# Performance work log

Hardware: AMD Instinct MI355X
Metric: run time of the kernel (lower is better)

Reference implementation:

```python
import jax, jax.numpy as jnp
import numpy as np


def setup_inputs() -> dict:
    key = jax.random.key(0)
    k = jax.random.split(key, 6)
    B, S, d, n = 4, 4096, 1024, 64
    x = jax.random.normal(k[0], (B, S, d), dtype=jnp.float32)
    gate_W = jax.random.normal(k[1], (d, n), dtype=jnp.float32) / np.sqrt(d).astype(np.float32)
    gate_b = jnp.full((n,), 3.0, dtype=jnp.float32)  # nn.init.constant_(gate_proj.bias, 3.0)
    B_W = jax.random.normal(k[2], (d, n), dtype=jnp.float32) / np.sqrt(d).astype(np.float32)
    C_W = jax.random.normal(k[3], (n, d), dtype=jnp.float32) / np.sqrt(n).astype(np.float32)
    out_W = jax.random.normal(k[4], (d, d), dtype=jnp.float32) / np.sqrt(d).astype(np.float32)
    mix_weight = jnp.eye(n, dtype=jnp.float32) + 0.01 * jax.random.normal(k[5], (n, n), dtype=jnp.float32)
    return {"x": x, "gate_W": gate_W, "gate_b": gate_b, "B_W": B_W,
            "C_W": C_W, "out_W": out_W, "mix_weight": mix_weight, "chunk_size": 16}


def _ssm_forward(x, gate_W, gate_b, B_W, C_W, out_W, mix_weight, chunk_size):
    Bb, S, d = x.shape
    n = gate_W.shape[1]
    C = chunk_size
    K = S // C  # seq_len chosen divisible by chunk_size -> F.pad path is a no-op
    # Vectorized per-timestep projections (done once for the whole sequence)
    gates = jax.nn.sigmoid(jnp.einsum('bsd,dn->bsn', x, gate_W) + gate_b)  # a_t in (0,1)
    b_all = jnp.einsum('bsd,dn->bsn', x, B_W)
    a_ch = gates.reshape(Bb, K, C, n).transpose(1, 2, 0, 3)  # (K, C, B, n)
    b_ch = b_all.reshape(Bb, K, C, n).transpose(1, 2, 0, 3)

    def chunk_step(h_prev, ab):
        a_c, b_c = ab  # each (C, B, n)
        def step(h, t):
            a_t, b_t = t
            h = a_t * h + b_t
            return h, h
        h_final, h_stack = jax.lax.scan(step, h_prev, (a_c, b_c))  # h_stack: (C, B, n)
        gate_prod = jnp.prod(a_c, axis=0)  # (B, n) cumulative diag gates
        # T_chunk = mix @ diag(gate_prod): T[b,i,j] = mix[i,j] * gate_prod[b,j]
        T = mix_weight[None, :, :] * gate_prod[:, None, :]
        Th = jnp.einsum('bij,bj->bi', T, h_prev)
        b_chunk = h_final - Th
        h_next = Th + b_chunk  # canonical inter-chunk propagation: T @ h_prev + b_chunk
        return h_next, h_stack

    h0 = jnp.zeros((Bb, n), dtype=x.dtype)
    _, h_all = jax.lax.scan(chunk_step, h0, (a_ch, b_ch))  # (K, C, B, n)
    h_seq = h_all.transpose(2, 0, 1, 3).reshape(Bb, S, n)
    y = jnp.einsum('bsn,nd->bsd', h_seq, C_W)
    out_gate = jax.nn.sigmoid(jnp.einsum('bsd,de->bse', x, out_W))
    return y * out_gate


def reference(x, gate_W, gate_b, B_W, C_W, out_W, mix_weight, chunk_size):
    return _ssm_forward(x, gate_W, gate_b, B_W, C_W, out_W, mix_weight, chunk_size)
```

## Files before the change

### kernel.cpp

```cpp
#include <hip/hip_runtime.h>
#include <stdint.h>

typedef __attribute__((ext_vector_type(8))) short short8;
typedef __attribute__((ext_vector_type(4))) float f32x4;
typedef __attribute__((ext_vector_type(4))) float f4;
typedef __attribute__((ext_vector_type(4))) unsigned short us4;

typedef unsigned short ushort_t;

__device__ __forceinline__ ushort_t f2bf(float f) {
    union { float f; uint32_t u; } c; c.f = f;
    uint32_t u = c.u;
    uint32_t r = u + 0x7fffu + ((u >> 16) & 1u);
    return (ushort_t)(r >> 16);
}
__device__ __forceinline__ float bf2f(ushort_t h) {
    union { uint32_t u; float f; } c; c.u = ((uint32_t)h) << 16;
    return c.f;
}

typedef const __attribute__((address_space(1))) unsigned int as1_uint;
typedef __attribute__((address_space(3))) unsigned int as3_uint;
__device__ __forceinline__ void gload_lds16(const void* g, void* l) {
    __builtin_amdgcn_global_load_lds((as1_uint*)g, (as3_uint*)l, 16, 0, 0);
}

#define SWIDX(r, c) ((r) * 64 + ((c) ^ (((r) & 7) << 3)))

__global__ void prep_weights(const float* __restrict__ gate_W, const float* __restrict__ B_W,
                             const float* __restrict__ C_W, const float* __restrict__ out_W,
                             ushort_t* __restrict__ W1t_hi, ushort_t* __restrict__ W1t_lo,
                             ushort_t* __restrict__ outWt, ushort_t* __restrict__ Ct)
{
    int idx = blockIdx.x * 256 + threadIdx.x;
    int stride = gridDim.x * 256;
    for (int i = idx; i < 1024 * 1024; i += stride) {
        int nn = i >> 10, kk = i & 1023;
        outWt[i] = f2bf(out_W[kk * 1024 + nn]);
    }
    for (int i = idx; i < 128 * 1024; i += stride) {
        int nn = i >> 10, kk = i & 1023;
        float v = (nn < 64) ? gate_W[kk * 64 + nn] : B_W[kk * 64 + (nn - 64)];
        ushort_t h = f2bf(v);
        W1t_hi[i] = h;
        W1t_lo[i] = f2bf(v - bf2f(h));
    }
    for (int i = idx; i < 1024 * 64; i += stride) {
        int nn = i >> 6, kk = i & 63;
        Ct[i] = f2bf(C_W[kk * 1024 + nn]);
    }
}

__global__ __launch_bounds__(256, 2)
void p1_kernel(const float* __restrict__ x,
               const ushort_t* __restrict__ W1t_hi, const ushort_t* __restrict__ W1t_lo,
               ushort_t* __restrict__ x_hi, float* __restrict__ Zpart)
{
    __shared__ ushort_t Ash[128 * 64];
    __shared__ ushort_t Asl[128 * 64];
    __shared__ ushort_t Bsh[64 * 64];
    __shared__ ushort_t Bsl[64 * 64];

    const int tid = threadIdx.x;
    const int wave = tid >> 6, lane = tid & 63;
    const int wm = wave >> 1, wn = wave & 1;
    const int s0 = blockIdx.x * 64;
    const int kc = blockIdx.y;

    f32x4 acc[4][2];
#pragma unroll
    for (int i = 0; i < 4; i++)
#pragma unroll
        for (int j = 0; j < 2; j++) { f32x4 z = {0.f,0.f,0.f,0.f}; acc[i][j] = z; }

    for (int kt = 0; kt < 8; ++kt) {
        const int k0 = kc * 512 + kt * 64;
#pragma unroll
        for (int p = 0; p < 4; ++p) {
            int c = p * 256 + wave * 64 + lane;
            int row = c >> 3, col = (c & 7) * 8;
            gload_lds16(W1t_hi + (size_t)row * 1024 + k0 + col,
                        &Ash[(p * 256 + wave * 64) * 8]);
            gload_lds16(W1t_lo + (size_t)row * 1024 + k0 + col,
                        &Asl[(p * 256 + wave * 64) * 8]);
        }
#pragma unroll
        for (int p = 0; p < 4; ++p) {
            int f = tid + p * 256;
            int row = f >> 4, col = (f & 15) * 4;
            f4 v = *(const f4*)(x + (size_t)(s0 + row) * 1024 + k0 + col);
            us4 hi, lo;
#pragma unroll
            for (int j = 0; j < 4; j++) {
                ushort_t h = f2bf(v[j]);
                hi[j] = h;
                lo[j] = f2bf(v[j] - bf2f(h));
            }
            *(us4*)&Bsh[row * 64 + col] = hi;
            *(us4*)&Bsl[row * 64 + col] = lo;
            *(us4*)(x_hi + (size_t)(s0 + row) * 1024 + k0 + col) = hi;
        }
        __syncthreads();
#pragma unroll
        for (int kk = 0; kk < 2; ++kk) {
            const int kb = kk * 32 + (lane >> 4) * 8;
            short8 ah[4], al[4], bh[2], bl[2];
#pragma unroll
            for (int fm = 0; fm < 4; fm++) {
                int r = wm * 64 + fm * 16 + (lane & 15);
                ah[fm] = *(const short8*)&Ash[r * 64 + kb];
                al[fm] = *(const short8*)&Asl[r * 64 + kb];
            }
#pragma unroll
            for (int fn = 0; fn < 2; fn++) {
                int r = wn * 32 + fn * 16 + (lane & 15);
                bh[fn] = *(const short8*)&Bsh[r * 64 + kb];
                bl[fn] = *(const short8*)&Bsl[r * 64 + kb];
            }
#pragma unroll
            for (int fm = 0; fm < 4; fm++)
#pragma unroll
                for (int fn = 0; fn < 2; fn++) {
                    acc[fm][fn] = __builtin_amdgcn_mfma_f32_16x16x32_bf16(ah[fm], bh[fn], acc[fm][fn], 0, 0, 0);
                    acc[fm][fn] = __builtin_amdgcn_mfma_f32_16x16x32_bf16(al[fm], bh[fn], acc[fm][fn], 0, 0, 0);
                    acc[fm][fn] = __builtin_amdgcn_mfma_f32_16x16x32_bf16(ah[fm], bl[fn], acc[fm][fn], 0, 0, 0);
                }
        }
        __syncthreads();
    }
#pragma unroll
    for (int fm = 0; fm < 4; fm++) {
#pragma unroll
        for (int fn = 0; fn < 2; fn++) {
            int scol = s0 + wn * 32 + fn * 16 + (lane & 15);
            int b = scol >> 12, sb = scol & 4095;
            int nbase = wm * 64 + fm * 16 + ((lane >> 4) << 2);
#pragma unroll
            for (int r = 0; r < 4; r++) {
                Zpart[((size_t)kc * 512 + b * 128 + nbase + r) * 4096 + sb] = acc[fm][fn][r];
            }
        }
    }
}

__global__ __launch_bounds__(256)
void scan_kernel(const float* __restrict__ Zpart, const float* __restrict__ gate_b,
                 ushort_t* __restrict__ hT)
{
    __shared__ float SA[256], SB[256];
    const int bn = blockIdx.x;
    const int t = threadIdx.x;
    const int b = bn >> 6, n = bn & 63;
    const float gb = gate_b[n];
    const float* g0 = Zpart + ((size_t)(b * 128 + n)) * 4096;
    const float* g1 = g0 + (size_t)512 * 4096;
    const float* b0 = Zpart + ((size_t)(b * 128 + 64 + n)) * 4096;
    const float* b1 = b0 + (size_t)512 * 4096;
    const int sb = t * 16;

    float a[16], bb[16];
#pragma unroll
    for (int q = 0; q < 4; q++) {
        f4 vg0 = *(const f4*)(g0 + sb + q * 4);
        f4 vg1 = *(const f4*)(g1 + sb + q * 4);
        f4 vb0 = *(const f4*)(b0 + sb + q * 4);
        f4 vb1 = *(const f4*)(b1 + sb + q * 4);
#pragma unroll
        for (int j = 0; j < 4; j++) {
            a[q * 4 + j] = 1.f / (1.f + __expf(-(vg0[j] + vg1[j] + gb)));
            bb[q * 4 + j] = vb0[j] + vb1[j];
        }
    }
    float A = 1.f, Bv = 0.f;
#pragma unroll
    for (int i = 0; i < 16; i++) { Bv = a[i] * Bv + bb[i]; A *= a[i]; }
    SA[t] = A; SB[t] = Bv;
    __syncthreads();
    for (int off = 1; off < 256; off <<= 1) {
        float a1 = 1.f, b1v = 0.f;
        if (t >= off) { a1 = SA[t - off]; b1v = SB[t - off]; }
        float a2 = SA[t], b2 = SB[t];
        __syncthreads();
        SA[t] = a1 * a2;
        SB[t] = a2 * b1v + b2;
        __syncthreads();
    }
    float h = (t == 0) ? 0.f : SB[t - 1];
    ushort_t ov[16];
#pragma unroll
    for (int i = 0; i < 16; i++) {
        h = a[i] * h + bb[i];
        ov[i] = f2bf(h);
    }
    ushort_t* dst = hT + (size_t)bn * 4096 + sb;
#pragma unroll
    for (int q = 0; q < 4; q++) {
        us4 o; o[0]=ov[q*4]; o[1]=ov[q*4+1]; o[2]=ov[q*4+2]; o[3]=ov[q*4+3];
        *(us4*)(dst + q * 4) = o;
    }
}

__global__ __launch_bounds__(512, 2)
void gemm_out256(const ushort_t* __restrict__ x_hi, const ushort_t* __restrict__ outWt,
                 const ushort_t* __restrict__ hT, const ushort_t* __restrict__ Ct,
                 float* __restrict__ out)
{
    __shared__ ushort_t As[2][256 * 64];
    __shared__ ushort_t Bs[2][256 * 64];

    const int tid = threadIdx.x;
    const int wave = tid >> 6, lane = tid & 63;
    const int wm = wave >> 2;
    const int wn = wave & 3;

    const int flat = blockIdx.x;
    const int swz = (flat & 7) * 32 + (flat >> 3);
    const int m0 = (swz >> 2) * 256;
    const int n0 = (swz & 3) * 256;

    const int lcol0 = (lane >> 4) * 8;
    const int lrow = lane & 15;
    const int lxor = (lrow & 7) << 3;

    const int aOff0 = (wm * 32 + lrow) * 64 + (lcol0 ^ lxor);
    const int aOff1 = (wm * 32 + lrow) * 64 + ((32 + lcol0) ^ lxor);
    const int bOff0 = (wn * 64 + lrow) * 64 + (lcol0 ^ lxor);
    const int bOff1 = (wn * 64 + lrow) * 64 + ((32 + lcol0) ^ lxor);

    const int rl0 = tid >> 3;
    const int col0 = ((tid & 7) ^ (rl0 & 7)) << 3;
    const ushort_t* gB0a = outWt + (size_t)(n0 + rl0) * 1024 + col0;
    const ushort_t* gB0b = gB0a + 64 * 1024;
    const ushort_t* gB1a = outWt + (size_t)(n0 + 128 + rl0) * 1024 + col0;
    const ushort_t* gB1b = gB1a + 64 * 1024;
    const ushort_t* gA0a = x_hi + (size_t)(m0 + rl0) * 1024 + col0;
    const ushort_t* gA0b = gA0a + 64 * 1024;
    const ushort_t* gA1a = x_hi + (size_t)(m0 + 128 + rl0) * 1024 + col0;
    const ushort_t* gA1b = gA1a + 64 * 1024;

    auto STG = [&](const ushort_t*& ga, const ushort_t*& gb, ushort_t* ldsbase) {
        gload_lds16(ga, ldsbase + wave * 512);
        gload_lds16(gb, ldsbase + 4096 + wave * 512);
        ga += 64; gb += 64;
    };

    f32x4 acc[8][4];
#pragma unroll
    for (int i = 0; i < 8; i++)
#pragma unroll
        for (int j = 0; j < 4; j++) { f32x4 z = {0.f,0.f,0.f,0.f}; acc[i][j] = z; }

    STG(gB0a, gB0b, &Bs[0][0]);
    STG(gB1a, gB1b, &Bs[0][8192]);
    STG(gA0a, gA0b, &As[0][0]);
    STG(gA1a, gA1b, &As[0][8192]);
    STG(gB0a, gB0b, &Bs[1][0]);
    STG(gB1a, gB1b, &Bs[1][8192]);
    STG(gA0a, gA0b, &As[1][0]);
    asm volatile("s_waitcnt vmcnt(6)" ::: "memory");
    __builtin_amdgcn_s_barrier();

    short8 aF[2][2], aN[2][2];
#pragma unroll
    for (int mm = 0; mm < 2; ++mm) {
        aF[mm][0] = *(const short8*)&As[0][aOff0 + mm * 1024];
        aF[mm][1] = *(const short8*)&As[0][aOff1 + mm * 1024];
    }

#define MFMA_Q(q)                                                                  \
    do {                                                                           \
        __builtin_amdgcn_s_setprio(1);                                             \
        _Pragma("unroll") for (int mm = 0; mm < 2; ++mm)                           \
            _Pragma("unroll") for (int fn = 0; fn < 4; ++fn) {                     \
                acc[2*(q)+mm][fn] = __builtin_amdgcn_mfma_f32_16x16x32_bf16(       \
                    aF[mm][0], bfr[fn][0], acc[2*(q)+mm][fn], 0, 0, 0);            \
                acc[2*(q)+mm][fn] = __builtin_amdgcn_mfma_f32_16x16x32_bf16(       \
                    aF[mm][1], bfr[fn][1], acc[2*(q)+mm][fn], 0, 0, 0);            \
            }                                                                      \
        __builtin_amdgcn_s_setprio(0);                                             \
    } while (0)

#define ACOPY()                                                                    \
    do { aF[0][0]=aN[0][0]; aF[0][1]=aN[0][1]; aF[1][0]=aN[1][0]; aF[1][1]=aN[1][1]; } while (0)

    for (int t = 0; t < 16; ++t) {
        const int bc = t & 1;
        const ushort_t* aP0 = &As[bc][aOff0];
        const ushort_t* aP1 = &As[bc][aOff1];
        const ushort_t* bP0 = &Bs[bc][bOff0];
        const ushort_t* bP1 = &Bs[bc][bOff1];
        const ushort_t* nA0 = &As[bc ^ 1][aOff0];
        const ushort_t* nA1 = &As[bc ^ 1][aOff1];
        short8 bfr[4][2];

        __builtin_amdgcn_s_barrier();
        if (t < 15) STG(gA1a, gA1b, &As[bc ^ 1][8192]);
#pragma unroll
        for (int fn = 0; fn < 4; ++fn) {
            bfr[fn][0] = *(const short8*)(bP0 + fn * 1024);
            bfr[fn][1] = *(const short8*)(bP1 + fn * 1024);
        }
#pragma unroll
        for (int mm = 0; mm < 2; ++mm) {
            aN[mm][0] = *(const short8*)(aP0 + 4096 + mm * 1024);
            aN[mm][1] = *(const short8*)(aP1 + 4096 + mm * 1024);
        }
        MFMA_Q(0);
        ACOPY();

        if (t < 15) { asm volatile("s_waitcnt vmcnt(8)" ::: "memory"); }
        else        { asm volatile("s_waitcnt vmcnt(0)" ::: "memory"); }
        __builtin_amdgcn_s_barrier();
        if (t < 14) STG(gB0a, gB0b, &Bs[bc][0]);
#pragma unroll
        for (int mm = 0; mm < 2; ++mm) {
            aN[mm][0] = *(const short8*)(aP0 + 2 * 4096 + mm * 1024);
            aN[mm][1] = *(const short8*)(aP1 + 2 * 4096 + mm * 1024);
        }
        MFMA_Q(1);
        ACOPY();

        __builtin_amdgcn_s_barrier();
        if (t < 14) STG(gB1a, gB1b, &Bs[bc][8192]);
#pragma unroll
        for (int mm = 0; mm < 2; ++mm) {
            aN[mm][0] = *(const short8*)(aP0 + 3 * 4096 + mm * 1024);
            aN[mm][1] = *(const short8*)(aP1 + 3 * 4096 + mm * 1024);
        }
        MFMA_Q(2);
        ACOPY();

        if (t < 14)       { asm volatile("s_waitcnt vmcnt(6)" ::: "memory"); }
        else if (t == 14) { asm volatile("s_waitcnt vmcnt(2)" ::: "memory"); }
        __builtin_amdgcn_s_barrier();
        if (t < 14) STG(gA0a, gA0b, &As[bc][0]);
        if (t < 15) {
#pragma unroll
            for (int mm = 0; mm < 2; ++mm) {
                aN[mm][0] = *(const short8*)(nA0 + mm * 1024);
                aN[mm][1] = *(const short8*)(nA1 + mm * 1024);
            }
        }
        MFMA_Q(3);
        if (t < 15) ACOPY();
    }
#undef MFMA_Q
#undef ACOPY

    const int b64 = (m0 >> 12) * 64;
    const int sb0 = m0 & 4095;
#pragma unroll
    for (int p = 0; p < 4; ++p) {
        int c = p * 512 + wave * 64 + lane;
        int row = c >> 3;
        int col = (((c & 7) ^ (row & 7)) << 3);
        gload_lds16(Ct + (size_t)(n0 + row) * 64 + col,
                    &Bs[0][(p * 512 + wave * 64) * 8]);
    }
#pragma unroll
    for (int p = 0; p < 4; ++p) {
        int c = tid + p * 512;
        int kn = c >> 5, mc = c & 31;
        short8 v = *(const short8*)(hT + (size_t)(b64 + kn) * 4096 + sb0 + mc * 8);
#pragma unroll
        for (int j = 0; j < 8; ++j)
            As[0][SWIDX(mc * 8 + j, kn)] = (ushort_t)v[j];
    }
    __syncthreads();

    short8 by[4][2];
#pragma unroll
    for (int fn = 0; fn < 4; fn++)
#pragma unroll
        for (int kk = 0; kk < 2; kk++) {
            int r = wn * 64 + fn * 16 + lrow;
            by[fn][kk] = *(const short8*)&Bs[0][SWIDX(r, kk * 32 + lcol0)];
        }

#pragma unroll
    for (int g = 0; g < 4; g++) {
        f32x4 ty[2][4];
#pragma unroll
        for (int mm = 0; mm < 2; mm++)
#pragma unroll
            for (int fn = 0; fn < 4; fn++) { f32x4 z = {0.f,0.f,0.f,0.f}; ty[mm][fn] = z; }
#pragma unroll
        for (int mm = 0; mm < 2; mm++) {
            int r = g * 64 + wm * 32 + mm * 16 + lrow;
            short8 a0 = *(const short8*)&As[0][SWIDX(r, lcol0)];
            short8 a1 = *(const short8*)&As[0][SWIDX(r, 32 + lcol0)];
#pragma unroll
            for (int fn = 0; fn < 4; fn++) {
                ty[mm][fn] = __builtin_amdgcn_mfma_f32_16x16x32_bf16(a0, by[fn][0], ty[mm][fn], 0, 0, 0);
                ty[mm][fn] = __builtin_amdgcn_mfma_f32_16x16x32_bf16(a1, by[fn][1], ty[mm][fn], 0, 0, 0);
            }
        }
#pragma unroll
        for (int mm = 0; mm < 2; mm++)
#pragma unroll
            for (int fn = 0; fn < 4; fn++) {
                int col = n0 + wn * 64 + fn * 16 + lrow;
                int rbase = m0 + g * 64 + wm * 32 + mm * 16 + ((lane >> 4) << 2);
#pragma unroll
                for (int r = 0; r < 4; r++) {
                    float og = 1.f / (1.f + __expf(-acc[g * 2 + mm][fn][r]));
                    out[(size_t)(rbase + r) * 1024 + col] = ty[mm][fn][r] * og;
                }
            }
    }
}

extern "C" void kernel_launch(void* const* d_in, const int* in_sizes, int n_in,
                              void* d_out, int out_size, void* d_ws, size_t ws_size,
                              hipStream_t stream)
{
    const float* x      = (const float*)d_in[0];
    const float* gate_W = (const float*)d_in[1];
    const float* gate_b = (const float*)d_in[2];
    const float* B_W    = (const float*)d_in[3];
    const float* C_W    = (const float*)d_in[4];
    const float* out_W  = (const float*)d_in[5];
    float* out = (float*)d_out;

    char* ws = (char*)d_ws;
    float*    Zpart  = (float*)(ws + 0);
    ushort_t* hT     = (ushort_t*)(ws + 16777216);
    ushort_t* x_hi   = (ushort_t*)(ws + 18874368);
    ushort_t* W1t_hi = (ushort_t*)(ws + 52428800);
    ushort_t* W1t_lo = (ushort_t*)(ws + 52690944);
    ushort_t* outWt  = (ushort_t*)(ws + 52953088);
    ushort_t* Ct     = (ushort_t*)(ws + 55050240);

    prep_weights<<<512, 256, 0, stream>>>(gate_W, B_W, C_W, out_W,
                                          W1t_hi, W1t_lo, outWt, Ct);

    p1_kernel<<<dim3(256, 2), 256, 0, stream>>>(x, W1t_hi, W1t_lo, x_hi, Zpart);

    scan_kernel<<<256, 256, 0, stream>>>(Zpart, gate_b, hT);

    gemm_out256<<<256, 512, 0, stream>>>(x_hi, outWt, hT, Ct, out);
}
```

Measured before the change: 99.55 us.

## Restructure GEMM main loop pipeline with one-stage prefetch and explicit barrier phases

Replaces the deeper prefetch schedule, which kept two LDS stages in flight and register-double-buffered the A fragments, with a simpler one-tile-ahead scheme. Each quarter now loads its fragments from LDS, issues the next tile's global->LDS loads into the other buffer, waits on lgkmcnt, and runs the MFMAs behind sched_barriers. The aim is to cut register pressure and make the ordering explicit. In exchange it adds more barriers per iteration and exposes LDS read latency before each MFMA group, since those reads are no longer overlapped.

```diff
diff --git a/kernel.cpp b/kernel.cpp
--- a/kernel.cpp
+++ b/kernel.cpp
@@ -254,18 +254,8 @@
     STG(gB1a, gB1b, &Bs[0][8192]);
     STG(gA0a, gA0b, &As[0][0]);
     STG(gA1a, gA1b, &As[0][8192]);
-    STG(gB0a, gB0b, &Bs[1][0]);
-    STG(gB1a, gB1b, &Bs[1][8192]);
-    STG(gA0a, gA0b, &As[1][0]);
-    asm volatile("s_waitcnt vmcnt(6)" ::: "memory");
+    asm volatile("s_waitcnt vmcnt(2)" ::: "memory");
     __builtin_amdgcn_s_barrier();
-
-    short8 aF[2][2], aN[2][2];
-#pragma unroll
-    for (int mm = 0; mm < 2; ++mm) {
-        aF[mm][0] = *(const short8*)&As[0][aOff0 + mm * 1024];
-        aF[mm][1] = *(const short8*)&As[0][aOff1 + mm * 1024];
-    }
 
 #define MFMA_Q(q)                                                                  \
     do {                                                                           \
@@ -273,79 +263,78 @@
         _Pragma("unroll") for (int mm = 0; mm < 2; ++mm)                           \
             _Pragma("unroll") for (int fn = 0; fn < 4; ++fn) {                     \
                 acc[2*(q)+mm][fn] = __builtin_amdgcn_mfma_f32_16x16x32_bf16(       \
-                    aF[mm][0], bfr[fn][0], acc[2*(q)+mm][fn], 0, 0, 0);            \
+                    afr[mm][0], bfr[fn][0], acc[2*(q)+mm][fn], 0, 0, 0);           \
                 acc[2*(q)+mm][fn] = __builtin_amdgcn_mfma_f32_16x16x32_bf16(       \
-                    aF[mm][1], bfr[fn][1], acc[2*(q)+mm][fn], 0, 0, 0);            \
+                    afr[mm][1], bfr[fn][1], acc[2*(q)+mm][fn], 0, 0, 0);           \
             }                                                                      \
         __builtin_amdgcn_s_setprio(0);                                             \
     } while (0)
 
-#define ACOPY()                                                                    \
-    do { aF[0][0]=aN[0][0]; aF[0][1]=aN[0][1]; aF[1][0]=aN[1][0]; aF[1][1]=aN[1][1]; } while (0)
-
     for (int t = 0; t < 16; ++t) {
         const int bc = t & 1;
-        const ushort_t* aP0 = &As[bc][aOff0];
-        const ushort_t* aP1 = &As[bc][aOff1];
-        const ushort_t* bP0 = &Bs[bc][bOff0];
-        const ushort_t* bP1 = &Bs[bc][bOff1];
-        const ushort_t* nA0 = &As[bc ^ 1][aOff0];
-        const ushort_t* nA1 = &As[bc ^ 1][aOff1];
-        short8 bfr[4][2];
-
-        __builtin_amdgcn_s_barrier();
+        const ushort_t* as = &As[bc][0];
+        const ushort_t* bs = &Bs[bc][0];
+        short8 bfr[4][2], afr[2][2];
+
+#pragma unroll
+        for (int fn = 0; fn < 4; ++fn) {
+            bfr[fn][0] = *(const short8*)(bs + bOff0 + fn * 1024);
+            bfr[fn][1] = *(const short8*)(bs + bOff1 + fn * 1024);
+        }
+#pragma unroll
+        for (int mm = 0; mm < 2; ++mm) {
+            afr[mm][0] = *(const short8*)(as + aOff0 + mm * 1024);
+            afr[mm][1] = *(const short8*)(as + aOff1 + mm * 1024);
+        }
+        if (t < 15) STG(gB0a, gB0b, &Bs[bc ^ 1][0]);
+        __builtin_amdgcn_s_barrier();
+        asm volatile("s_waitcnt lgkmcnt(0)" ::: "memory");
+        __builtin_amdgcn_sched_barrier(0);
+        MFMA_Q(0);
+        __builtin_amdgcn_s_barrier();
+
+#pragma unroll
+        for (int mm = 0; mm < 2; ++mm) {
+            afr[mm][0] = *(const short8*)(as + aOff0 + 4096 + mm * 1024);
+            afr[mm][1] = *(const short8*)(as + aOff1 + 4096 + mm * 1024);
+        }
+        if (t < 15) {
+            STG(gB1a, gB1b, &Bs[bc ^ 1][8192]);
+            STG(gA0a, gA0b, &As[bc ^ 1][0]);
+        }
+        __builtin_amdgcn_s_barrier();
+        asm volatile("s_waitcnt lgkmcnt(0)" ::: "memory");
+        __builtin_amdgcn_sched_barrier(0);
+        MFMA_Q(1);
+        if (t < 15) { asm volatile("s_waitcnt vmcnt(6)" ::: "memory"); }
+        else        { asm volatile("s_waitcnt vmcnt(0)" ::: "memory"); }
+        __builtin_amdgcn_s_barrier();
+
+#pragma unroll
+        for (int mm = 0; mm < 2; ++mm) {
+            afr[mm][0] = *(const short8*)(as + aOff0 + 2 * 4096 + mm * 1024);
+            afr[mm][1] = *(const short8*)(as + aOff1 + 2 * 4096 + mm * 1024);
+        }
         if (t < 15) STG(gA1a, gA1b, &As[bc ^ 1][8192]);
-#pragma unroll
-        for (int fn = 0; fn < 4; ++fn) {
-            bfr[fn][0] = *(const short8*)(bP0 + fn * 1024);
-            bfr[fn][1] = *(const short8*)(bP1 + fn * 1024);
-        }
+        __builtin_amdgcn_s_barrier();
+        asm volatile("s_waitcnt lgkmcnt(0)" ::: "memory");
+        __builtin_amdgcn_sched_barrier(0);
+        MFMA_Q(2);
+        __builtin_amdgcn_s_barrier();
+
 #pragma unroll
         for (int mm = 0; mm < 2; ++mm) {
-            aN[mm][0] = *(const short8*)(aP0 + 4096 + mm * 1024);
-            aN[mm][1] = *(const short8*)(aP1 + 4096 + mm * 1024);
-        }
-        MFMA_Q(0);
-        ACOPY();
-
-        if (t < 15) { asm volatile("s_waitcnt vmcnt(8)" ::: "memory"); }
-        else        { asm volatile("s_waitcnt vmcnt(0)" ::: "memory"); }
-        __builtin_amdgcn_s_barrier();
-        if (t < 14) STG(gB0a, gB0b, &Bs[bc][0]);
-#pragma unroll
-        for (int mm = 0; mm < 2; ++mm) {
-            aN[mm][0] = *(const short8*)(aP0 + 2 * 4096 + mm * 1024);
-            aN[mm][1] = *(const short8*)(aP1 + 2 * 4096 + mm * 1024);
-        }
-        MFMA_Q(1);
-        ACOPY();
-
-        __builtin_amdgcn_s_barrier();
-        if (t < 14) STG(gB1a, gB1b, &Bs[bc][8192]);
-#pragma unroll
-        for (int mm = 0; mm < 2; ++mm) {
-            aN[mm][0] = *(const short8*)(aP0 + 3 * 4096 + mm * 1024);
-            aN[mm][1] = *(const short8*)(aP1 + 3 * 4096 + mm * 1024);
-        }
-        MFMA_Q(2);
-        ACOPY();
-
-        if (t < 14)       { asm volatile("s_waitcnt vmcnt(6)" ::: "memory"); }
-        else if (t == 14) { asm volatile("s_waitcnt vmcnt(2)" ::: "memory"); }
-        __builtin_amdgcn_s_barrier();
-        if (t < 14) STG(gA0a, gA0b, &As[bc][0]);
-        if (t < 15) {
-#pragma unroll
-            for (int mm = 0; mm < 2; ++mm) {
-                aN[mm][0] = *(const short8*)(nA0 + mm * 1024);
-                aN[mm][1] = *(const short8*)(nA1 + mm * 1024);
-            }
-        }
+            afr[mm][0] = *(const short8*)(as + aOff0 + 3 * 4096 + mm * 1024);
+            afr[mm][1] = *(const short8*)(as + aOff1 + 3 * 4096 + mm * 1024);
+        }
+        __builtin_amdgcn_s_barrier();
+        asm volatile("s_waitcnt lgkmcnt(0)" ::: "memory");
+        __builtin_amdgcn_sched_barrier(0);
         MFMA_Q(3);
-        if (t < 15) ACOPY();
+        if (t < 15) { asm volatile("s_waitcnt vmcnt(2)" ::: "memory"); }
+        __builtin_amdgcn_s_barrier();
     }
 #undef MFMA_Q
-#undef ACOPY
 
     const int b64 = (m0 >> 12) * 64;
     const int sb0 = m0 & 4095;
```

Result: faster. 96.32 us (-3.2%).
